# Performance work log

Measured on AMD Instinct MI355X. Metric: run time of the kernel, lower is better.

The kernel has to match this reference:

```python
import jax, jax.numpy as jnp
import numpy as np

B, NBAND, C, T = 2, 40, 64, 1500
NUM_CODE = 1024


def setup_inputs() -> dict:
    key = jax.random.key(0)
    k1, k2 = jax.random.split(key)
    x = jax.random.normal(k1, (B, NBAND, C, T), dtype=jnp.float32)
    # layer_idx == 0 init: unit-norm codes per band
    cb = jax.random.normal(k2, (NBAND, NUM_CODE, C), dtype=jnp.float32)
    eps = jnp.finfo(jnp.float32).eps
    cb = cb / jnp.sqrt(jnp.sum(cb * cb, axis=-1, keepdims=True) + eps)
    return {"x": x, "codebook": cb}


def reference(x, codebook):
    batch, nband, nchan, time = x.shape
    num_code = codebook.shape[1]
    # x.detach().permute(0,3,1,2).view(B*T, nband, nchan)
    xd = jax.lax.stop_gradient(x).transpose(0, 3, 1, 2).reshape(batch * time, nband, nchan)
    dist = (
        jnp.sum(xd * xd, axis=-1, keepdims=True)
        + jnp.sum(codebook * codebook, axis=-1)
        - 2.0 * jnp.einsum("nbc,bkc->nbk", xd, codebook)
    )
    min_idx = jnp.argmin(dist, axis=-1)  # [BT, nband]
    # per-band gather: quantized[n, b] = codebook[b, min_idx[n, b]]
    quantized = codebook[jnp.arange(nband)[None, :], min_idx]  # [BT, nband, nchan]
    # view(B, T, nband, nchan).permute(0,2,3,1)
    return quantized.reshape(batch, time, nband, nchan).transpose(0, 2, 3, 1)
```

## Files before the change

kernel.cpp:

```cpp
#include <hip/hip_runtime.h>


#define NBAND  40
#define CH     64
#define TT     1500
#define NCODE  1024
#define MT     128
#define PAD    68
#define THRESH 1e-3f

typedef short v8s __attribute__((ext_vector_type(8)));
typedef float v4f __attribute__((ext_vector_type(4)));

#define CBF_USHORTS ((size_t)NBAND * 32 * 8 * 64 * 8)
#define CBF_BYTES   (CBF_USHORTS * 2)
#define WS_NEEDED   (CBF_BYTES + (size_t)NBAND * NCODE * 4)

__device__ __forceinline__ unsigned short f2bf(float f) {
    unsigned u = __float_as_uint(f);
    return (unsigned short)((u + 0x7FFFu + ((u >> 16) & 1u)) >> 16);
}
__device__ __forceinline__ float bf2f(unsigned short h) {
    return __uint_as_float(((unsigned)h) << 16);
}
__device__ __forceinline__ unsigned ford(float f) {
    unsigned u = __float_as_uint(f);
    return (u & 0x80000000u) ? ~u : (u | 0x80000000u);
}
__device__ __forceinline__ unsigned long long packsk(float f, unsigned k) {
    return ((unsigned long long)ford(f) << 32) | (unsigned long long)k;
}

typedef __attribute__((address_space(1))) const unsigned char* gas_p;
typedef __attribute__((address_space(3))) unsigned char*       las_p;
__device__ __forceinline__ void async_ld16(const void* g, void* l) {
    __builtin_amdgcn_global_load_lds((gas_p)g, (las_p)l, 16, 0, 0);
}

__global__ __launch_bounds__(256)
void vq_prep(const float* __restrict__ cb,
             unsigned short* __restrict__ CBF,
             float* __restrict__ C2) {
    const int band = blockIdx.y;
    const int g    = blockIdx.x * 4 + (threadIdx.x >> 6);
    const int lane = threadIdx.x & 63;
    const int col  = lane & 15;
    const int quad = lane >> 4;

    float sq[2] = {0.f, 0.f};
    #pragma unroll
    for (int l = 0; l < 4; ++l) {
        const int ni = l >> 1, ks = l & 1;
        const int code = g * 32 + ni * 16 + col;
        const int c0   = ks * 32 + quad * 8;
        const float* src = cb + ((size_t)(band * NCODE + code)) * CH + c0;
        const float4 v0 = *(const float4*)src;
        const float4 v1 = *(const float4*)(src + 4);
        const float vv[8] = {v0.x, v0.y, v0.z, v0.w, v1.x, v1.y, v1.z, v1.w};
        union { unsigned short u[8]; v8s v; } hh, ll;
        #pragma unroll
        for (int j = 0; j < 8; ++j) {
            const unsigned short h = f2bf(vv[j]);
            hh.u[j] = h;
            ll.u[j] = f2bf(vv[j] - bf2f(h));
            sq[ni] = fmaf(vv[j], vv[j], sq[ni]);
        }
        const size_t gb = (size_t)(band * 32 + g) * 8;
        *(v8s*)&CBF[(gb + l)     * 512 + lane * 8] = hh.v;
        *(v8s*)&CBF[(gb + 4 + l) * 512 + lane * 8] = ll.v;
    }
    #pragma unroll
    for (int ni = 0; ni < 2; ++ni) {
        sq[ni] += __shfl_xor(sq[ni], 16);
        sq[ni] += __shfl_xor(sq[ni], 32);
    }
    if (quad == 0) {
        C2[band * NCODE + g * 32 + col]      = sq[0];
        C2[band * NCODE + g * 32 + 16 + col] = sq[1];
    }
}

__global__ __launch_bounds__(256, 4)
void vq_main(const float* __restrict__ x,
             const float* __restrict__ cb,
             const unsigned short* __restrict__ CBF,
             const float* __restrict__ C2f,
             float* __restrict__ out) {
    __shared__ alignas(16) unsigned char SMEM[MT * PAD * 2 * 2];
    __shared__ float c2_s[NCODE];
    __shared__ unsigned long long best_s[MT];
    __shared__ unsigned amb_s[4];
    __shared__ float xrow_s[CH];

    unsigned short* XH_s = (unsigned short*)SMEM;
    unsigned short* XL_s = XH_s + MT * PAD;

    const int tile  = blockIdx.x;
    const int band  = blockIdx.y;
    const int batch = blockIdx.z;
    const int t0    = tile * MT;

    const int tid  = threadIdx.x;
    const int wave = tid >> 6;
    const int lane = tid & 63;
    const int quad = lane >> 4;
    const int col  = lane & 15;

    if (tid < 4) amb_s[tid] = 0u;
    {
        const float* src = C2f + band * NCODE;
        #pragma unroll
        for (int i = 0; i < 4; ++i) c2_s[tid + 256 * i] = src[tid + 256 * i];
    }
    {
        const int c = tid & 63;
        const int g = tid >> 6;
        const float* src = x + ((size_t)(batch * NBAND + band) * CH + c) * TT + t0;
        #pragma unroll
        for (int i = 0; i < 8; ++i) {
            const int t = (g + 4 * i) * 4;
            float4 v = make_float4(0.f, 0.f, 0.f, 0.f);
            if (t0 + t + 3 < TT) v = *(const float4*)(src + t);
            const float vv[4] = {v.x, v.y, v.z, v.w};
            #pragma unroll
            for (int j = 0; j < 4; ++j) {
                const unsigned short h = f2bf(vv[j]);
                XH_s[(t + j) * PAD + c] = h;
                XL_s[(t + j) * PAD + c] = f2bf(vv[j] - bf2f(h));
            }
        }
    }
    __syncthreads();

    v8s ah[2][2], al[2][2];
    #pragma unroll
    for (int mi = 0; mi < 2; ++mi)
        #pragma unroll
        for (int ks = 0; ks < 2; ++ks) {
            const int off = (wave * 32 + mi * 16 + col) * PAD + ks * 32 + quad * 8;
            ah[mi][ks] = *(const v8s*)&XH_s[off];
            al[mi][ks] = *(const v8s*)&XL_s[off];
        }
    __syncthreads();

    float m1[8], m2[8];
    int   id8[8];
    #pragma unroll
    for (int i = 0; i < 8; ++i) { m1[i] = 3.4028235e38f; m2[i] = 3.4028235e38f; id8[i] = 0x7fffffff; }

    const unsigned short* fbase = CBF + (size_t)(band * 32) * 4096 + (size_t)lane * 8;
    unsigned short* LBUF = (unsigned short*)SMEM;

    auto stage_group = [&](int g, int buf) {
        #pragma unroll
        for (int i = 0; i < 2; ++i) {
            const int p = wave * 2 + i;
            async_ld16(fbase + (size_t)g * 4096 + p * 512,
                       LBUF + (size_t)buf * 4096 + p * 512);
        }
    };

    stage_group(0, 0);

    for (int g = 0; g < 32; ++g) {
        __syncthreads();
        if (g + 1 < 32) stage_group(g + 1, (g + 1) & 1);

        const unsigned short* lb = LBUF + (size_t)(g & 1) * 4096 + lane * 8;
        v4f acc[2][2];
        #pragma unroll
        for (int mi = 0; mi < 2; ++mi)
            #pragma unroll
            for (int ni = 0; ni < 2; ++ni) acc[mi][ni] = (v4f){0.f, 0.f, 0.f, 0.f};

        #pragma unroll
        for (int ks = 0; ks < 2; ++ks) {
            const v8s bh0 = *(const v8s*)(lb + (0 * 2 + ks) * 512);
            const v8s bh1 = *(const v8s*)(lb + (1 * 2 + ks) * 512);
            const v8s bl0 = *(const v8s*)(lb + (4 + 0 * 2 + ks) * 512);
            const v8s bl1 = *(const v8s*)(lb + (4 + 1 * 2 + ks) * 512);
            #pragma unroll
            for (int mi = 0; mi < 2; ++mi) {
                acc[mi][0] = __builtin_amdgcn_mfma_f32_16x16x32_bf16(ah[mi][ks], bh0, acc[mi][0], 0, 0, 0);
                acc[mi][1] = __builtin_amdgcn_mfma_f32_16x16x32_bf16(ah[mi][ks], bh1, acc[mi][1], 0, 0, 0);
            }
            #pragma unroll
            for (int mi = 0; mi < 2; ++mi) {
                acc[mi][0] = __builtin_amdgcn_mfma_f32_16x16x32_bf16(ah[mi][ks], bl0, acc[mi][0], 0, 0, 0);
                acc[mi][1] = __builtin_amdgcn_mfma_f32_16x16x32_bf16(ah[mi][ks], bl1, acc[mi][1], 0, 0, 0);
            }
            #pragma unroll
            for (int mi = 0; mi < 2; ++mi) {
                acc[mi][0] = __builtin_amdgcn_mfma_f32_16x16x32_bf16(al[mi][ks], bh0, acc[mi][0], 0, 0, 0);
                acc[mi][1] = __builtin_amdgcn_mfma_f32_16x16x32_bf16(al[mi][ks], bh1, acc[mi][1], 0, 0, 0);
            }
        }
        #pragma unroll
        for (int ni = 0; ni < 2; ++ni) {
            const float c2v = c2_s[g * 32 + ni * 16 + col];
            const int   kg  = g * 32 + ni * 16 + col;
            #pragma unroll
            for (int mi = 0; mi < 2; ++mi)
                #pragma unroll
                for (int r = 0; r < 4; ++r) {
                    const int j = mi * 4 + r;
                    const float s = fmaf(-2.f, acc[mi][ni][r], c2v);
                    m2[j] = fminf(m2[j], fmaxf(s, m1[j]));
                    const bool lt = s < m1[j];
                    m1[j]  = lt ? s : m1[j];
                    id8[j] = lt ? kg : id8[j];
                }
        }
    }
    __syncthreads();

    float* RM1 = (float*)SMEM;
    float* RM2 = RM1 + MT * 16;
    int*   RI  = (int*)(RM2 + MT * 16);
    #pragma unroll
    for (int j = 0; j < 8; ++j) {
        const int t = wave * 32 + (j >> 2) * 16 + quad * 4 + (j & 3);
        RM1[t * 16 + col] = m1[j];
        RM2[t * 16 + col] = m2[j];
        RI [t * 16 + col] = id8[j];
    }
    __syncthreads();

    if (tid < MT) {
        const int t = tid;
        float M1 = RM1[t * 16], M2 = RM2[t * 16];
        int   I  = RI[t * 16];
        #pragma unroll
        for (int j = 1; j < 16; ++j) {
            const float a1 = RM1[t * 16 + j];
            const float a2 = RM2[t * 16 + j];
            const int   ai = RI [t * 16 + j];
            if (a1 < M1 || (a1 == M1 && ai < I)) { M2 = fminf(M2, M1); M1 = a1; I = ai; }
            else                                  { M2 = fminf(M2, a1); }
            M2 = fminf(M2, a2);
        }
        best_s[t] = packsk(M1, (unsigned)I);
        if ((M2 - M1) <= THRESH && t0 + t < TT)
            atomicOr(&amb_s[t >> 5], 1u << (t & 31));
    }
    __syncthreads();

    for (int t = 0; t < MT; ++t) {
        if ((amb_s[t >> 5] >> (t & 31)) & 1u) {
            if (tid < CH) xrow_s[tid] = x[((size_t)(batch * NBAND + band) * CH + tid) * TT + t0 + t];
            if (tid == CH) best_s[t] = ~0ULL;
            __syncthreads();
            #pragma unroll
            for (int i = 0; i < 4; ++i) {
                const int k = tid * 4 + i;
                const float* crow = cb + ((size_t)(band * NCODE + k)) * CH;
                float dot = 0.f, c2e = 0.f;
                #pragma unroll 8
                for (int c = 0; c < CH; ++c) {
                    const float cv = crow[c];
                    dot = fmaf(cv, xrow_s[c], dot);
                    c2e = fmaf(cv, cv, c2e);
                }
                atomicMin(&best_s[t], packsk(fmaf(-2.f, dot, c2e), (unsigned)k));
            }
            __syncthreads();
        }
    }
    __syncthreads();

    {
        const int tloc  = tid & 127;
        const int chalf = tid >> 7;
        if (t0 + tloc < TT) {
            const unsigned idx = (unsigned)(best_s[tloc] & 0xFFFFFFFFull) & (NCODE - 1);
            const float* crow = cb + ((size_t)(band * NCODE + idx)) * CH;
            float* ob = out + ((size_t)(batch * NBAND + band) * CH) * TT + t0 + tloc;
            #pragma unroll
            for (int i = 0; i < 32; ++i) {
                const int c = chalf * 32 + i;
                ob[(size_t)c * TT] = crow[c];
            }
        }
    }
}

#define TN 128
#define KC 128
__global__ __launch_bounds__(256, 2)
void vq_fp32_kernel(const float* __restrict__ x,
                    const float* __restrict__ cb,
                    float* __restrict__ out) {
    __shared__ float XT_s[CH * TN];
    __shared__ float CBT_s[CH * KC];
    __shared__ float c2part[256];
    const int tile = blockIdx.x, band = blockIdx.y, batch = blockIdx.z;
    const int t0 = tile * TN;
    const int tid = threadIdx.x;
    const int tx = tid & 15, ty = tid >> 4;
    {
        const int c = tid >> 2, q = tid & 3;
        const float* src = x + ((size_t)(batch * NBAND + band) * CH + c) * TT + t0;
        #pragma unroll
        for (int i = 0; i < 8; ++i) {
            const int t = q * 32 + i * 4;
            float4 v = make_float4(0.f, 0.f, 0.f, 0.f);
            if (t0 + t < TT) v = *(const float4*)(src + t);
            *(float4*)&XT_s[c * TN + t] = v;
        }
    }
    float vmin[8]; int vidx[8];
    #pragma unroll
    for (int i = 0; i < 8; ++i) { vmin[i] = 3.4e38f; vidx[i] = 0x7fffffff; }
    for (int kc = 0; kc < NCODE; kc += KC) {
        __syncthreads();
        {
            const int k = tid >> 1, ch0 = (tid & 1) * 32;
            const float* src = cb + ((size_t)(band * NCODE + kc + k)) * CH + ch0;
            float s = 0.f;
            #pragma unroll
            for (int i = 0; i < 8; ++i) {
                const float4 v = *(const float4*)(src + i * 4);
                const int c0 = ch0 + i * 4;
                CBT_s[(c0 + 0) * KC + k] = v.x; CBT_s[(c0 + 1) * KC + k] = v.y;
                CBT_s[(c0 + 2) * KC + k] = v.z; CBT_s[(c0 + 3) * KC + k] = v.w;
                s = fmaf(v.x, v.x, s); s = fmaf(v.y, v.y, s);
                s = fmaf(v.z, v.z, s); s = fmaf(v.w, v.w, s);
            }
            c2part[tid] = s;
        }
        __syncthreads();
        float acc[8][8];
        #pragma unroll
        for (int ii = 0; ii < 8; ++ii)
            #pragma unroll
            for (int jj = 0; jj < 8; ++jj) acc[ii][jj] = 0.f;
        #pragma unroll 4
        for (int c = 0; c < CH; ++c) {
            const float4 xa0 = *(const float4*)&XT_s[c * TN + tx * 4];
            const float4 xa1 = *(const float4*)&XT_s[c * TN + 64 + tx * 4];
            const float4 cv0 = *(const float4*)&CBT_s[c * KC + ty * 4];
            const float4 cv1 = *(const float4*)&CBT_s[c * KC + 64 + ty * 4];
            const float xa[8] = {xa0.x, xa0.y, xa0.z, xa0.w, xa1.x, xa1.y, xa1.z, xa1.w};
            const float cv[8] = {cv0.x, cv0.y, cv0.z, cv0.w, cv1.x, cv1.y, cv1.z, cv1.w};
            #pragma unroll
            for (int ii = 0; ii < 8; ++ii)
                #pragma unroll
                for (int jj = 0; jj < 8; ++jj) acc[ii][jj] = fmaf(xa[ii], cv[jj], acc[ii][jj]);
        }
        #pragma unroll
        for (int jj = 0; jj < 8; ++jj) {
            const int kl = (jj < 4) ? (ty * 4 + jj) : (64 + ty * 4 + (jj - 4));
            const float c2v = c2part[2 * kl] + c2part[2 * kl + 1];
            const int kglob = kc + kl;
            #pragma unroll
            for (int ii = 0; ii < 8; ++ii) {
                const float score = fmaf(-2.f, acc[ii][jj], c2v);
                if (score < vmin[ii]) { vmin[ii] = score; vidx[ii] = kglob; }
            }
        }
    }
    __syncthreads();
    float* redv = XT_s;
    int* redi = (int*)(XT_s + TN * 16);
    int* idxs = (int*)(XT_s + TN * 32);
    #pragma unroll
    for (int ii = 0; ii < 8; ++ii) {
        const int t = (ii < 4) ? (tx * 4 + ii) : (64 + tx * 4 + (ii - 4));
        redv[t * 16 + ty] = vmin[ii];
        redi[t * 16 + ty] = vidx[ii];
    }
    __syncthreads();
    if (tid < TN) {
        float bv = redv[tid * 16]; int bi = redi[tid * 16];
        #pragma unroll
        for (int j = 1; j < 16; ++j) {
            const float v = redv[tid * 16 + j]; const int id = redi[tid * 16 + j];
            if (v < bv || (v == bv && id < bi)) { bv = v; bi = id; }
        }
        idxs[tid] = bi;
    }
    __syncthreads();
    {
        const int tloc = tid & 127, chalf = tid >> 7;
        if (t0 + tloc < TT) {
            const int idx = idxs[tloc];
            const float* crow = cb + ((size_t)(band * NCODE + idx)) * CH;
            float* ob = out + ((size_t)(batch * NBAND + band) * CH) * TT + t0 + tloc;
            #pragma unroll
            for (int i = 0; i < 32; ++i) {
                const int c = chalf * 32 + i;
                ob[(size_t)c * TT] = crow[c];
            }
        }
    }
}

extern "C" void kernel_launch(void* const* d_in, const int* in_sizes, int n_in,
                              void* d_out, int out_size, void* d_ws, size_t ws_size,
                              hipStream_t stream) {
    const float* x  = (const float*)d_in[0];
    const float* cb = (const float*)d_in[1];
    float* out = (float*)d_out;
    dim3 grid((TT + MT - 1) / MT, NBAND, 2);
    if (ws_size >= WS_NEEDED) {
        unsigned short* CBF = (unsigned short*)d_ws;
        float* C2 = (float*)((char*)d_ws + CBF_BYTES);
        vq_prep<<<dim3(8, NBAND), dim3(256), 0, stream>>>(cb, CBF, C2);
        vq_main<<<grid, dim3(256), 0, stream>>>(x, cb, CBF, C2, out);
    } else {
        vq_fp32_kernel<<<grid, dim3(256), 0, stream>>>(x, cb, out);
    }
}
```

Baseline: 215.3 us.

## Stream codebook fragments via register double-buffering, stage output gather through LDS

Result: no change. 216.3 us (+0.5%).

```diff
diff --git a/kernel.cpp b/kernel.cpp
--- a/kernel.cpp
+++ b/kernel.cpp
@@ -30,11 +30,12 @@
 __device__ __forceinline__ unsigned long long packsk(float f, unsigned k) {
     return ((unsigned long long)ford(f) << 32) | (unsigned long long)k;
 }
-
-typedef __attribute__((address_space(1))) const unsigned char* gas_p;
-typedef __attribute__((address_space(3))) unsigned char*       las_p;
-__device__ __forceinline__ void async_ld16(const void* g, void* l) {
-    __builtin_amdgcn_global_load_lds((gas_p)g, (las_p)l, 16, 0, 0);
+__device__ __forceinline__ float med3f(float a, float b, float c) {
+#if __has_builtin(__builtin_amdgcn_fmed3f)
+    return __builtin_amdgcn_fmed3f(a, b, c);
+#else
+    return fminf(fmaxf(a, b), c);
+#endif
 }
 
 __global__ __launch_bounds__(256)
@@ -80,7 +81,7 @@
     }
 }
 
-__global__ __launch_bounds__(256, 4)
+__global__ __launch_bounds__(256, 3)
 void vq_main(const float* __restrict__ x,
              const float* __restrict__ cb,
              const unsigned short* __restrict__ CBF,
@@ -148,37 +149,18 @@
     #pragma unroll
     for (int i = 0; i < 8; ++i) { m1[i] = 3.4028235e38f; m2[i] = 3.4028235e38f; id8[i] = 0x7fffffff; }
 
-    const unsigned short* fbase = CBF + (size_t)(band * 32) * 4096 + (size_t)lane * 8;
-    unsigned short* LBUF = (unsigned short*)SMEM;
-
-    auto stage_group = [&](int g, int buf) {
-        #pragma unroll
-        for (int i = 0; i < 2; ++i) {
-            const int p = wave * 2 + i;
-            async_ld16(fbase + (size_t)g * 4096 + p * 512,
-                       LBUF + (size_t)buf * 4096 + p * 512);
-        }
-    };
-
-    stage_group(0, 0);
-
-    for (int g = 0; g < 32; ++g) {
-        __syncthreads();
-        if (g + 1 < 32) stage_group(g + 1, (g + 1) & 1);
-
-        const unsigned short* lb = LBUF + (size_t)(g & 1) * 4096 + lane * 8;
+    const unsigned short* fb = CBF + (size_t)(band * 32) * 4096 + (size_t)lane * 8;
+
+    auto compute = [&](const v8s (&buf)[8], int g) {
         v4f acc[2][2];
         #pragma unroll
         for (int mi = 0; mi < 2; ++mi)
             #pragma unroll
             for (int ni = 0; ni < 2; ++ni) acc[mi][ni] = (v4f){0.f, 0.f, 0.f, 0.f};
-
         #pragma unroll
         for (int ks = 0; ks < 2; ++ks) {
-            const v8s bh0 = *(const v8s*)(lb + (0 * 2 + ks) * 512);
-            const v8s bh1 = *(const v8s*)(lb + (1 * 2 + ks) * 512);
-            const v8s bl0 = *(const v8s*)(lb + (4 + 0 * 2 + ks) * 512);
-            const v8s bl1 = *(const v8s*)(lb + (4 + 1 * 2 + ks) * 512);
+            const v8s bh0 = buf[0 * 2 + ks], bh1 = buf[2 + ks];
+            const v8s bl0 = buf[4 + ks],     bl1 = buf[6 + ks];
             #pragma unroll
             for (int mi = 0; mi < 2; ++mi) {
                 acc[mi][0] = __builtin_amdgcn_mfma_f32_16x16x32_bf16(ah[mi][ks], bh0, acc[mi][0], 0, 0, 0);
@@ -205,12 +187,29 @@
                 for (int r = 0; r < 4; ++r) {
                     const int j = mi * 4 + r;
                     const float s = fmaf(-2.f, acc[mi][ni][r], c2v);
-                    m2[j] = fminf(m2[j], fmaxf(s, m1[j]));
+                    m2[j] = med3f(s, m1[j], m2[j]);
                     const bool lt = s < m1[j];
                     m1[j]  = lt ? s : m1[j];
                     id8[j] = lt ? kg : id8[j];
                 }
         }
+    };
+
+    v8s bufA[8], bufB[8];
+    #pragma unroll
+    for (int p = 0; p < 8; ++p) bufA[p] = *(const v8s*)(fb + p * 512);
+
+    for (int g = 0; g < 32; g += 2) {
+        const unsigned short* nf = fb + (size_t)(g + 1) * 4096;
+        #pragma unroll
+        for (int p = 0; p < 8; ++p) bufB[p] = *(const v8s*)(nf + p * 512);
+        compute(bufA, g);
+        if (g + 2 < 32) {
+            const unsigned short* nf2 = fb + (size_t)(g + 2) * 4096;
+            #pragma unroll
+            for (int p = 0; p < 8; ++p) bufA[p] = *(const v8s*)(nf2 + p * 512);
+        }
+        compute(bufB, g + 1);
     }
     __syncthreads();
 
@@ -269,16 +268,22 @@
     __syncthreads();
 
     {
+        float* OT = (float*)SMEM;
+        #pragma unroll
+        for (int r = 0; r < MT; r += 4) {
+            const int row = r + wave;
+            const unsigned idx = (unsigned)(best_s[row] & 0xFFFFFFFFull) & (NCODE - 1);
+            OT[row * 67 + lane] = cb[((size_t)(band * NCODE + idx)) * CH + lane];
+        }
+        __syncthreads();
         const int tloc  = tid & 127;
         const int chalf = tid >> 7;
         if (t0 + tloc < TT) {
-            const unsigned idx = (unsigned)(best_s[tloc] & 0xFFFFFFFFull) & (NCODE - 1);
-            const float* crow = cb + ((size_t)(band * NCODE + idx)) * CH;
             float* ob = out + ((size_t)(batch * NBAND + band) * CH) * TT + t0 + tloc;
             #pragma unroll
             for (int i = 0; i < 32; ++i) {
                 const int c = chalf * 32 + i;
-                ob[(size_t)c * TT] = crow[c];
+                ob[(size_t)c * TT] = OT[tloc * 67 + c];
             }
         }
     }
```
